# Performance work log

Hardware: AMD Instinct MI355X
Metric: run time of the kernel (lower is better)

Reference implementation:

```python
import jax, jax.numpy as jnp
import numpy as np

EMBED_DIM = 1024
NUM_HEADS = 16
HEAD_DIM = EMBED_DIM // NUM_HEADS
R = 16
LORA_ALPHA = 32
SCALING = LORA_ALPHA / R


def setup_inputs() -> dict:
    key = jax.random.key(0)
    ks = jax.random.split(key, 16)
    S, B, E = 2048, 4, EMBED_DIM
    def n(k, shape, scale=1.0):
        return jax.random.normal(k, shape, dtype=jnp.float32) * scale
    return {
        "x_q": n(ks[0], (S, B, E)),
        "x_k": n(ks[1], (S, B, E)),
        "x_v": n(ks[2], (S, B, E)),
        "Wq": n(ks[3], (E, E), 0.02),
        "bq": n(ks[4], (E,), 0.02),
        "Aq": n(ks[5], (E, R), 0.02),
        "Bq": n(ks[6], (R, E), 0.02),
        "Wk": n(ks[7], (E, E), 0.02),
        "bk": n(ks[8], (E,), 0.02),
        "Wv": n(ks[9], (E, E), 0.02),
        "bv": n(ks[10], (E,), 0.02),
        "Av": n(ks[11], (E, R), 0.02),
        "Bv": n(ks[12], (R, E), 0.02),
        "Wo": n(ks[13], (E, E), 0.02),
        "bo": n(ks[14], (E,), 0.02),
    }


def _lora_linear(x, W, b, A, B):
    # F.linear(x, W, b) + (x @ A) @ B * scaling
    return x @ W.T + b + ((x @ A) @ B) * SCALING


def reference(x_q, x_k, x_v, Wq, bq, Aq, Bq, Wk, bk, Wv, bv, Av, Bv, Wo, bo):
    S, Bsz, E = x_q.shape
    H, D = NUM_HEADS, HEAD_DIM
    q = _lora_linear(x_q, Wq, bq, Aq, Bq)      # [S, B, E]
    k = x_k @ Wk.T + bk                          # [S, B, E]
    v = _lora_linear(x_v, Wv, bv, Av, Bv)
    # [S, B, E] -> [B*H, S, D]
    q = q.reshape(S, Bsz * H, D).transpose(1, 0, 2)
    k = k.reshape(S, Bsz * H, D).transpose(1, 0, 2)
    v = v.reshape(S, Bsz * H, D).transpose(1, 0, 2)
    scores = jnp.einsum('nsd,ntd->nst', q, k) / (D ** 0.5)  # [B*H, S, S]
    attn = jax.nn.softmax(scores, axis=-1)
    out = jnp.einsum('nst,ntd->nsd', attn, v)                # [B*H, S, D]
    out = out.transpose(1, 0, 2).reshape(S, Bsz, E)
    return out @ Wo.T + bo
```

## Files before the change

### kernel.cpp

```cpp
#include <hip/hip_runtime.h>
#include <stdint.h>

#define S_LEN 2048
#define BSZ   4
#define EMB   1024
#define NH    16
#define HD    64
#define NHEADS (BSZ*NH)
#define M_ROWS (S_LEN*BSZ)
#define R_LORA 16

typedef unsigned short u16t;
typedef __bf16 bf16x8 __attribute__((ext_vector_type(8)));
typedef float  f32x4  __attribute__((ext_vector_type(4)));
typedef float  f32x16 __attribute__((ext_vector_type(16)));
typedef unsigned int uint2v __attribute__((ext_vector_type(2)));

#define QSCALE (0.125f * 1.44269504089f)

__device__ __forceinline__ u16t f2bf(float f){
  union { float f; uint32_t u; } v; v.f = f;
  uint32_t u = v.u;
  u += 0x7FFFu + ((u >> 16) & 1u);
  return (u16t)(u >> 16);
}

__device__ __forceinline__ uint32_t cvtpk(float a, float b){
  uint32_t r;
  asm("v_cvt_pk_bf16_f32 %0, %1, %2" : "=v"(r) : "v"(a), "v"(b));
  return r;
}

__device__ __forceinline__ void gload16(const void* g, void* l){
  __builtin_amdgcn_global_load_lds(
    (const __attribute__((address_space(1))) unsigned int*)g,
    (__attribute__((address_space(3))) unsigned int*)l, 16, 0, 0);
}

__device__ __forceinline__ int swz(int b){ return b ^ (((b >> 7) & 7) << 4); }

__global__ __launch_bounds__(256) void k_wprep4(
    const float* __restrict__ Wq, const float* __restrict__ Aq, const float* __restrict__ Bq,
    const float* __restrict__ Wk,
    const float* __restrict__ Wv, const float* __restrict__ Av, const float* __restrict__ Bv,
    const float* __restrict__ Wo,
    u16t* __restrict__ oq, u16t* __restrict__ ok, u16t* __restrict__ ov, u16t* __restrict__ oo){
  int which = blockIdx.y;
  const float* W = which==0?Wq : which==1?Wk : which==2?Wv : Wo;
  u16t* out      = which==0?oq : which==1?ok : which==2?ov : oo;
  int n = blockIdx.x, t = threadIdx.x;
  float4 wv = reinterpret_cast<const float4*>(W + (size_t)n*EMB)[t];
  float add[4] = {0.f, 0.f, 0.f, 0.f};
  if (which == 0 || which == 2){
    const float* A_ = which==0 ? Aq : Av;
    const float* B_ = which==0 ? Bq : Bv;
    float bcol[16];
    #pragma unroll
    for (int r = 0; r < 16; r++) bcol[r] = 2.0f * B_[(size_t)r*EMB + n];
    #pragma unroll
    for (int j = 0; j < 4; j++){
      const float4* ar = reinterpret_cast<const float4*>(A_ + (size_t)(4*t+j)*R_LORA);
      float4 a0 = ar[0], a1 = ar[1], a2 = ar[2], a3 = ar[3];
      add[j] = a0.x*bcol[0] + a0.y*bcol[1] + a0.z*bcol[2] + a0.w*bcol[3]
             + a1.x*bcol[4] + a1.y*bcol[5] + a1.z*bcol[6] + a1.w*bcol[7]
             + a2.x*bcol[8] + a2.y*bcol[9] + a2.z*bcol[10]+ a2.w*bcol[11]
             + a3.x*bcol[12]+ a3.y*bcol[13]+ a3.z*bcol[14]+ a3.w*bcol[15];
    }
  }
  float scale = (which == 0) ? QSCALE : 1.0f;
  ushort4 o = { f2bf((wv.x+add[0])*scale), f2bf((wv.y+add[1])*scale),
                f2bf((wv.z+add[2])*scale), f2bf((wv.w+add[3])*scale) };
  reinterpret_cast<ushort4*>(out + (size_t)n*EMB)[t] = o;
}

__global__ __launch_bounds__(256) void k_cvt3(
    const float* __restrict__ xq, const float* __restrict__ xk, const float* __restrict__ xv,
    u16t* __restrict__ oq, u16t* __restrict__ ok, u16t* __restrict__ ov){
  const float* x = blockIdx.y==0 ? xq : blockIdx.y==1 ? xk : xv;
  u16t* o        = blockIdx.y==0 ? oq : blockIdx.y==1 ? ok : ov;
  const int n = M_ROWS*EMB;
  int stride = gridDim.x * 256 * 4;
  for (int i = (blockIdx.x*256 + threadIdx.x)*4; i < n; i += stride){
    float4 v = *reinterpret_cast<const float4*>(x + i);
    ushort4 u = { f2bf(v.x), f2bf(v.y), f2bf(v.z), f2bf(v.w) };
    *reinterpret_cast<ushort4*>(o + i) = u;
  }
}

__device__ __forceinline__ void gemm_main(
    const u16t* __restrict__ Abase, const u16t* __restrict__ Bbase,
    u16t* smem, int t, int wr, int wc, int l15, int lg, f32x4 (&acc)[4][4]){
  int k0 = 0;
  auto stage = [&](int buf){
    u16t* d = smem + buf*16384;
    #pragma unroll
    for (int i = 0; i < 4; i++){
      int c = i*256 + t;
      int row = c >> 3, ch = c & 7;
      int srcch = ch ^ (row & 7);
      gload16(Abase + (size_t)row*EMB + k0 + srcch*8, d + c*8);
    }
    #pragma unroll
    for (int i = 0; i < 4; i++){
      int c = i*256 + t;
      int row = c >> 3, ch = c & 7;
      int srcch = ch ^ (row & 7);
      gload16(Bbase + (size_t)row*EMB + k0 + srcch*8, d + 8192 + c*8);
    }
    k0 += 64;
  };

  stage(0);
  __syncthreads();

  const int NK = EMB/64;
  for (int kt = 0; kt < NK; ++kt){
    int cur = kt & 1;
    if (kt+1 < NK) stage(cur^1);
    const char* Abuf = (const char*)(smem + cur*16384);
    const char* Bbuf = Abuf + 16384;
    #pragma unroll
    for (int kk = 0; kk < 2; kk++){
      bf16x8 af[4], bfr[4];
      #pragma unroll
      for (int i = 0; i < 4; i++){
        af[i]  = *reinterpret_cast<const bf16x8*>(
            Abuf + swz((wr*64 + i*16 + l15)*128 + kk*64 + lg*16));
        bfr[i] = *reinterpret_cast<const bf16x8*>(
            Bbuf + swz((wc*64 + i*16 + l15)*128 + kk*64 + lg*16));
      }
      __builtin_amdgcn_s_setprio(1);
      #pragma unroll
      for (int mi = 0; mi < 4; mi++)
        #pragma unroll
        for (int ni = 0; ni < 4; ni++)
          acc[mi][ni] = __builtin_amdgcn_mfma_f32_16x16x32_bf16(af[mi], bfr[ni], acc[mi][ni], 0, 0, 0);
      __builtin_amdgcn_s_setprio(0);
    }
    __syncthreads();
  }
}

__global__ __launch_bounds__(256) void k_gemm_qkv(
    const u16t* __restrict__ xqb, const u16t* __restrict__ xkb, const u16t* __restrict__ xvb,
    const u16t* __restrict__ Wqb, const u16t* __restrict__ Wkb, const u16t* __restrict__ Wvb,
    const float* __restrict__ bq, const float* __restrict__ bk, const float* __restrict__ bv,
    u16t* __restrict__ q_att, u16t* __restrict__ k_att, u16t* __restrict__ vT)
{
  __shared__ u16t smem[2*16384];
  int z = blockIdx.z;
  const u16t* A  = z==0 ? xqb : z==1 ? xkb : xvb;
  const u16t* Bw = z==0 ? Wqb : z==1 ? Wkb : Wvb;
  const float* bias = z==0 ? bq : z==1 ? bk : bv;
  float bscale = z==0 ? QSCALE : 1.0f;
  u16t* att = z==0 ? q_att : z==1 ? k_att : vT;

  int t = threadIdx.x;
  int lane = t & 63, w = t >> 6;
  int wr = w >> 1, wc = w & 1;
  int l15 = lane & 15, lg = lane >> 4;
  int m0 = blockIdx.x * 128;
  int n0 = blockIdx.y * 128;

  f32x4 acc[4][4];
  #pragma unroll
  for (int i = 0; i < 4; i++)
    #pragma unroll
    for (int j = 0; j < 4; j++)
      acc[i][j] = (f32x4){0.f, 0.f, 0.f, 0.f};

  gemm_main(A + (size_t)m0*EMB, Bw + (size_t)n0*EMB, smem, t, wr, wc, l15, lg, acc);

  float bval[4];
  #pragma unroll
  for (int ni = 0; ni < 4; ni++)
    bval[ni] = bias[n0 + wc*64 + ni*16 + l15] * bscale;

  if (z < 2){
    #pragma unroll
    for (int mi = 0; mi < 4; mi++)
      #pragma unroll
      for (int ni = 0; ni < 4; ni++)
        #pragma unroll
        for (int j = 0; j < 4; j++){
          int m_local = wr*64 + mi*16 + lg*4 + j;
          int n_local = wc*64 + ni*16 + l15;
          *(u16t*)((char*)smem + swz(m_local*256 + n_local*2)) = f2bf(acc[mi][ni][j] + bval[ni]);
        }
    __syncthreads();
    #pragma unroll
    for (int i = 0; i < 8; i++){
      int c = i*256 + t;
      int m_local = c >> 4, nch = c & 15;
      uint4 val = *(const uint4*)((const char*)smem + swz(m_local*256 + nch*16));
      int m = m0 + m_local;
      int s = m >> 2, b = m & 3;
      int n = n0 + nch*8;
      int h = n >> 6, d = n & 63;
      *(uint4*)&att[(size_t)((b*NH + h)*S_LEN + s)*HD + d] = val;
    }
  } else {
    #pragma unroll
    for (int mi = 0; mi < 4; mi++)
      #pragma unroll
      for (int ni = 0; ni < 4; ni++)
        #pragma unroll
        for (int j = 0; j < 4; j++){
          int m_local = wr*64 + mi*16 + lg*4 + j;
          int n_local = wc*64 + ni*16 + l15;
          *(u16t*)((char*)smem + swz(n_local*256 + m_local*2)) = f2bf(acc[mi][ni][j] + bval[ni]);
        }
    __syncthreads();
    #pragma unroll
    for (int i = 0; i < 8; i++){
      int u = i*256 + t;
      int dl = u >> 4, b = (u >> 2) & 3, sc = u & 3;
      u16t tmp[8];
      #pragma unroll
      for (int z2 = 0; z2 < 8; z2++)
        tmp[z2] = *(const u16t*)((const char*)smem + swz(dl*256 + ((sc*8+z2)*4 + b)*2));
      int n_glob = n0 + dl;
      int h = n_glob >> 6, d = n_glob & 63;
      int s0 = (m0 >> 2) + sc*8;
      *(uint4*)&att[((size_t)((b*NH + h)*HD + d))*S_LEN + s0] = *(const uint4*)tmp;
    }
  }
}

__global__ __launch_bounds__(256) void k_gemm_o(
    const u16t* __restrict__ A, const u16t* __restrict__ Bw,
    const float* __restrict__ bias, float* __restrict__ Cout)
{
  __shared__ u16t smem[2*16384];
  int t = threadIdx.x;
  int lane = t & 63, w = t >> 6;
  int wr = w >> 1, wc = w & 1;
  int l15 = lane & 15, lg = lane >> 4;
  int m0 = blockIdx.x * 128;
  int n0 = blockIdx.y * 128;

  f32x4 acc[4][4];
  #pragma unroll
  for (int i = 0; i < 4; i++)
    #pragma unroll
    for (int j = 0; j < 4; j++)
      acc[i][j] = (f32x4){0.f, 0.f, 0.f, 0.f};

  gemm_main(A + (size_t)m0*EMB, Bw + (size_t)n0*EMB, smem, t, wr, wc, l15, lg, acc);

  float bval[4];
  #pragma unroll
  for (int ni = 0; ni < 4; ni++)
    bval[ni] = bias[n0 + wc*64 + ni*16 + l15];

  #pragma unroll
  for (int mi = 0; mi < 4; mi++){
    #pragma unroll
    for (int j = 0; j < 4; j++){
      int m = m0 + wr*64 + mi*16 + lg*4 + j;
      #pragma unroll
      for (int ni = 0; ni < 4; ni++){
        int n = n0 + wc*64 + ni*16 + l15;
        Cout[(size_t)m*EMB + n] = acc[mi][ni][j] + bval[ni];
      }
    }
  }
}

__global__ __launch_bounds__(256) void k_attn(
    const u16t* __restrict__ Qa, const u16t* __restrict__ Ka,
    const u16t* __restrict__ VTa, u16t* __restrict__ Oa)
{
  __shared__ u16t smem[2*8192];
  int t = threadIdx.x;
  int lane = t & 63, w = t >> 6;
  int l31 = lane & 31, hi = lane >> 5;
  int head = blockIdx.x;
  int qw = blockIdx.y*128 + w*32;
  const u16t* Qh = Qa + (size_t)head * S_LEN * HD;
  const char* Khc = (const char*)(Ka + (size_t)head * S_LEN * HD);
  const char* VTc = (const char*)(VTa + (size_t)head * HD * S_LEN);

  bf16x8 qf[4];
  #pragma unroll
  for (int ds = 0; ds < 4; ds++)
    qf[ds] = *reinterpret_cast<const bf16x8*>(
        Qh + (size_t)(qw + l31)*HD + ds*16 + hi*8);

  bf16x8 ones;
  { union { uint32_t u[4]; bf16x8 v; } o;
    o.u[0]=o.u[1]=o.u[2]=o.u[3]=0x3F803F80u; ones = o.v; }

  f32x16 oacc[2], lacc;
  oacc[0] = (f32x16)(0.f); oacc[1] = (f32x16)(0.f); lacc = (f32x16)(0.f);

  auto stage = [&](int buf, int key0){
    char* Kd = (char*)smem + buf*16384;
    char* Vd = Kd + 8192;
    #pragma unroll
    for (int i = 0; i < 2; i++){
      int c = i*256 + t;
      gload16(Khc + (size_t)key0*128 + swz(c*16), Kd + c*16);
    }
    #pragma unroll
    for (int i = 0; i < 2; i++){
      int c = i*256 + t;
      int tb = swz(c*16);
      gload16(VTc + (size_t)(tb>>7)*(S_LEN*2) + key0*2 + (tb&127), Vd + c*16);
    }
  };

  stage(0, 0);
  __syncthreads();

  const int NT = S_LEN/64;
  for (int nt = 0; nt < NT; ++nt){
    int cur = nt & 1;
    if (nt+1 < NT) stage(cur^1, (nt+1)*64);
    const char* Kb = (const char*)smem + cur*16384;
    const char* Vb = Kb + 8192;

    f32x16 sacc[2];
    sacc[0] = (f32x16)(0.f); sacc[1] = (f32x16)(0.f);
    __builtin_amdgcn_s_setprio(1);
    #pragma unroll
    for (int blk = 0; blk < 2; blk++){
      #pragma unroll
      for (int ds = 0; ds < 4; ds++){
        bf16x8 kf = *reinterpret_cast<const bf16x8*>(Kb + swz((blk*32 + l31)*128 + ds*32 + hi*16));
        sacc[blk] = __builtin_amdgcn_mfma_f32_32x32x16_bf16(kf, qf[ds], sacc[blk], 0,0,0);
      }
    }
    __builtin_amdgcn_s_setprio(0);

    #pragma unroll
    for (int blk = 0; blk < 2; blk++)
      #pragma unroll
      for (int r = 0; r < 16; r++)
        sacc[blk][r] = __builtin_amdgcn_exp2f(sacc[blk][r]);

    bf16x8 pa[4];
    #pragma unroll
    for (int blk = 0; blk < 2; blk++){
      #pragma unroll
      for (int kl = 0; kl < 2; kl++){
        union { uint32_t u[4]; bf16x8 v; } fr;
        #pragma unroll
        for (int i = 0; i < 2; i++){
          uint32_t x = cvtpk(sacc[blk][kl*8 + 2*i],     sacc[blk][kl*8 + 2*i + 1]);
          uint32_t y = cvtpk(sacc[blk][kl*8 + 4 + 2*i], sacc[blk][kl*8 + 4 + 2*i + 1]);
          uint2v r = __builtin_amdgcn_permlane32_swap(x, y, false, false);
          fr.u[i]   = r.x;
          fr.u[i+2] = r.y;
        }
        pa[blk*2 + kl] = fr.v;
      }
    }

    __builtin_amdgcn_s_setprio(1);
    #pragma unroll
    for (int dblk = 0; dblk < 2; dblk++){
      #pragma unroll
      for (int ks = 0; ks < 4; ks++){
        bf16x8 vf = *reinterpret_cast<const bf16x8*>(Vb + swz((dblk*32 + l31)*128 + ks*32 + hi*16));
        oacc[dblk] = __builtin_amdgcn_mfma_f32_32x32x16_bf16(vf, pa[ks], oacc[dblk], 0,0,0);
      }
    }
    #pragma unroll
    for (int ks = 0; ks < 4; ks++)
      lacc = __builtin_amdgcn_mfma_f32_32x32x16_bf16(ones, pa[ks], lacc, 0,0,0);
    __builtin_amdgcn_s_setprio(0);
    __syncthreads();
  }

  float inv = 1.0f / lacc[0];
  #pragma unroll
  for (int dblk = 0; dblk < 2; dblk++){
    #pragma unroll
    for (int rp = 0; rp < 8; rp++){
      int reg = 2*rp;
      int d = dblk*32 + (reg&3) + 8*(reg>>2) + 4*hi;
      uint32_t wv = cvtpk(oacc[dblk][reg]*inv, oacc[dblk][reg+1]*inv);
      *(uint32_t*)((char*)smem + swz((w*32 + l31)*128 + d*2)) = wv;
    }
  }
  __syncthreads();
  int b = head >> 4, h = head & 15;
  #pragma unroll
  for (int i = 0; i < 4; i++){
    int c = i*256 + t;
    int row = c >> 3;
    int col = c & 7;
    uint4 val = *(const uint4*)((const char*)smem + swz(row*128 + col*16));
    int q = blockIdx.y*128 + row;
    *(uint4*)(Oa + (size_t)(q*BSZ + b)*EMB + h*HD + col*8) = val;
  }
}

extern "C" void kernel_launch(void* const* d_in, const int* in_sizes, int n_in,
                              void* d_out, int out_size, void* d_ws, size_t ws_size,
                              hipStream_t stream) {
  const float* x_q = (const float*)d_in[0];
  const float* x_k = (const float*)d_in[1];
  const float* x_v = (const float*)d_in[2];
  const float* Wq  = (const float*)d_in[3];
  const float* bq  = (const float*)d_in[4];
  const float* Aq  = (const float*)d_in[5];
  const float* Bq  = (const float*)d_in[6];
  const float* Wk  = (const float*)d_in[7];
  const float* bk  = (const float*)d_in[8];
  const float* Wv  = (const float*)d_in[9];
  const float* bv  = (const float*)d_in[10];
  const float* Av  = (const float*)d_in[11];
  const float* Bv  = (const float*)d_in[12];
  const float* Wo  = (const float*)d_in[13];
  const float* bo  = (const float*)d_in[14];
  float* out = (float*)d_out;

  char* ws = (char*)d_ws;
  size_t off = 0;
  auto alloc = [&](size_t bytes){
    void* p = ws + off; off += (bytes + 255) & ~(size_t)255; return p;
  };
  u16t* xqb   = (u16t*)alloc((size_t)M_ROWS*EMB*2);
  u16t* xkb   = (u16t*)alloc((size_t)M_ROWS*EMB*2);
  u16t* xvb   = (u16t*)alloc((size_t)M_ROWS*EMB*2);
  u16t* q_att = (u16t*)alloc((size_t)M_ROWS*EMB*2);
  u16t* k_att = (u16t*)alloc((size_t)M_ROWS*EMB*2);
  u16t* vT    = (u16t*)alloc((size_t)M_ROWS*EMB*2);
  u16t* Wqb = (u16t*)alloc((size_t)EMB*EMB*2);
  u16t* Wkb = (u16t*)alloc((size_t)EMB*EMB*2);
  u16t* Wvb = (u16t*)alloc((size_t)EMB*EMB*2);
  u16t* Wob = (u16t*)alloc((size_t)EMB*EMB*2);
  (void)ws_size; (void)in_sizes; (void)n_in; (void)out_size;

  k_wprep4<<<dim3(EMB, 4), 256, 0, stream>>>(Wq, Aq, Bq, Wk, Wv, Av, Bv, Wo,
                                             Wqb, Wkb, Wvb, Wob);
  k_cvt3<<<dim3(2048, 3), 256, 0, stream>>>(x_q, x_k, x_v, xqb, xkb, xvb);

  k_gemm_qkv<<<dim3(M_ROWS/128, EMB/128, 3), 256, 0, stream>>>(
      xqb, xkb, xvb, Wqb, Wkb, Wvb, bq, bk, bv, q_att, k_att, vT);

  k_attn<<<dim3(NHEADS, S_LEN/128), 256, 0, stream>>>(q_att, k_att, vT, xqb);

  k_gemm_o<<<dim3(M_ROWS/128, EMB/128), 256, 0, stream>>>(xqb, Wob, bo, out);
}
```

Before: 235.3 us.

## Rewrite QKV GEMM as 256x256-tile, 8-wave kernel with interleaved LDS pipeline

Replaces the 128x128, 4-wave QKV projection GEMM with a 256x256-tile, 512-thread kernel that uses 128 KB of dynamic LDS for double-buffered A/B tiles. The main loop interleaves fragment loads, MFMA batches and the next tile's global-to-LDS loads, using raw s_barrier and vmcnt waits instead of __syncthreads. Block indices are remapped to a swizzled order. The larger tile raises arithmetic intensity and overlaps loads with compute, at the cost of fewer blocks (384), higher register pressure and reliance on hand-placed waitcnt counts for correctness. The shared gemm_main helper is inlined into the output-projection kernel, which is otherwise unchanged.

```diff
diff --git a/kernel.cpp b/kernel.cpp
--- a/kernel.cpp
+++ b/kernel.cpp
@@ -17,6 +17,10 @@
 typedef unsigned int uint2v __attribute__((ext_vector_type(2)));
 
 #define QSCALE (0.125f * 1.44269504089f)
+
+#define BARRIER_RAW  asm volatile("s_barrier" ::: "memory")
+#define VMCNT8       asm volatile("s_waitcnt vmcnt(8)" ::: "memory")
+#define VMCNT0       asm volatile("s_waitcnt vmcnt(0)" ::: "memory")
 
 __device__ __forceinline__ u16t f2bf(float f){
   union { float f; uint32_t u; } v; v.f = f;
@@ -87,142 +91,178 @@
   }
 }
 
-__device__ __forceinline__ void gemm_main(
-    const u16t* __restrict__ Abase, const u16t* __restrict__ Bbase,
-    u16t* smem, int t, int wr, int wc, int l15, int lg, f32x4 (&acc)[4][4]){
-  int k0 = 0;
-  auto stage = [&](int buf){
-    u16t* d = smem + buf*16384;
-    #pragma unroll
-    for (int i = 0; i < 4; i++){
-      int c = i*256 + t;
-      int row = c >> 3, ch = c & 7;
-      int srcch = ch ^ (row & 7);
-      gload16(Abase + (size_t)row*EMB + k0 + srcch*8, d + c*8);
-    }
-    #pragma unroll
-    for (int i = 0; i < 4; i++){
-      int c = i*256 + t;
-      int row = c >> 3, ch = c & 7;
-      int srcch = ch ^ (row & 7);
-      gload16(Bbase + (size_t)row*EMB + k0 + srcch*8, d + 8192 + c*8);
-    }
-    k0 += 64;
-  };
-
-  stage(0);
-  __syncthreads();
-
-  const int NK = EMB/64;
-  for (int kt = 0; kt < NK; ++kt){
-    int cur = kt & 1;
-    if (kt+1 < NK) stage(cur^1);
-    const char* Abuf = (const char*)(smem + cur*16384);
-    const char* Bbuf = Abuf + 16384;
-    #pragma unroll
-    for (int kk = 0; kk < 2; kk++){
-      bf16x8 af[4], bfr[4];
-      #pragma unroll
-      for (int i = 0; i < 4; i++){
-        af[i]  = *reinterpret_cast<const bf16x8*>(
-            Abuf + swz((wr*64 + i*16 + l15)*128 + kk*64 + lg*16));
-        bfr[i] = *reinterpret_cast<const bf16x8*>(
-            Bbuf + swz((wc*64 + i*16 + l15)*128 + kk*64 + lg*16));
-      }
-      __builtin_amdgcn_s_setprio(1);
-      #pragma unroll
-      for (int mi = 0; mi < 4; mi++)
-        #pragma unroll
-        for (int ni = 0; ni < 4; ni++)
-          acc[mi][ni] = __builtin_amdgcn_mfma_f32_16x16x32_bf16(af[mi], bfr[ni], acc[mi][ni], 0, 0, 0);
-      __builtin_amdgcn_s_setprio(0);
-    }
-    __syncthreads();
-  }
-}
-
-__global__ __launch_bounds__(256) void k_gemm_qkv(
+__global__ __launch_bounds__(512, 2) void k_gemm_qkv8(
     const u16t* __restrict__ xqb, const u16t* __restrict__ xkb, const u16t* __restrict__ xvb,
     const u16t* __restrict__ Wqb, const u16t* __restrict__ Wkb, const u16t* __restrict__ Wvb,
     const float* __restrict__ bq, const float* __restrict__ bk, const float* __restrict__ bv,
     u16t* __restrict__ q_att, u16t* __restrict__ k_att, u16t* __restrict__ vT)
 {
-  __shared__ u16t smem[2*16384];
-  int z = blockIdx.z;
-  const u16t* A  = z==0 ? xqb : z==1 ? xkb : xvb;
-  const u16t* Bw = z==0 ? Wqb : z==1 ? Wkb : Wvb;
-  const float* bias = z==0 ? bq : z==1 ? bk : bv;
-  float bscale = z==0 ? QSCALE : 1.0f;
-  u16t* att = z==0 ? q_att : z==1 ? k_att : vT;
+  extern __shared__ u16t smem[];
+  int lin = blockIdx.x + 32*(blockIdx.y + 4*blockIdx.z);
+  int nl  = (lin & 7)*48 + (lin >> 3);
+  int bx = nl & 31, rest = nl >> 5;
+  int by = rest & 3, bz = rest >> 2;
+
+  const u16t* Ap = bz==0 ? xqb : bz==1 ? xkb : xvb;
+  const u16t* Bp = bz==0 ? Wqb : bz==1 ? Wkb : Wvb;
+  const float* bias = bz==0 ? bq : bz==1 ? bk : bv;
+  float bscale = bz==0 ? QSCALE : 1.0f;
 
   int t = threadIdx.x;
-  int lane = t & 63, w = t >> 6;
-  int wr = w >> 1, wc = w & 1;
+  int lane = t & 63, wid = t >> 6;
+  int wr = wid >> 2, wc = wid & 3;
   int l15 = lane & 15, lg = lane >> 4;
-  int m0 = blockIdx.x * 128;
-  int n0 = blockIdx.y * 128;
-
-  f32x4 acc[4][4];
-  #pragma unroll
-  for (int i = 0; i < 4; i++)
+  int m0 = bx * 256;
+  int n0 = by * 256;
+  const u16t* Ag = Ap + (size_t)m0*EMB;
+  const u16t* Bg = Bp + (size_t)n0*EMB;
+
+  auto stageA = [&](int buf, int k, int h){
+    const u16t* src = Ag + (size_t)(h*128)*EMB + k*64;
+    char* dst = (char*)smem + buf*65536 + h*16384;
+    #pragma unroll
+    for (int i = 0; i < 2; i++){
+      int c = i*512 + t;
+      int row = c >> 3, ch = c & 7;
+      gload16(src + (size_t)row*EMB + (ch ^ (row & 7))*8, dst + c*16);
+    }
+  };
+  auto stageB = [&](int buf, int k, int h){
+    const u16t* src = Bg + (size_t)(h*128)*EMB + k*64;
+    char* dst = (char*)smem + buf*65536 + 32768 + h*16384;
+    #pragma unroll
+    for (int i = 0; i < 2; i++){
+      int c = i*512 + t;
+      int row = c >> 3, ch = c & 7;
+      gload16(src + (size_t)row*EMB + (ch ^ (row & 7))*8, dst + c*16);
+    }
+  };
+
+  f32x4 acc[8][4];
+  #pragma unroll
+  for (int i = 0; i < 8; i++)
     #pragma unroll
     for (int j = 0; j < 4; j++)
       acc[i][j] = (f32x4){0.f, 0.f, 0.f, 0.f};
 
-  gemm_main(A + (size_t)m0*EMB, Bw + (size_t)n0*EMB, smem, t, wr, wc, l15, lg, acc);
+  bf16x8 af[4][2];
+  bf16x8 bfr[4][2];
+
+  auto ldA = [&](int buf, int miBase){
+    const char* base = (const char*)smem + buf*65536 + wr*16384;
+    #pragma unroll
+    for (int m2 = 0; m2 < 4; m2++)
+      #pragma unroll
+      for (int kk = 0; kk < 2; kk++)
+        af[m2][kk] = *reinterpret_cast<const bf16x8*>(
+            base + swz(((miBase+m2)*16 + l15)*128 + kk*64 + lg*16));
+  };
+  auto ldB2 = [&](int buf, int niBase){
+    const char* base = (const char*)smem + buf*65536 + 32768 + (wc>>1)*16384;
+    #pragma unroll
+    for (int n2 = 0; n2 < 2; n2++)
+      #pragma unroll
+      for (int kk = 0; kk < 2; kk++)
+        bfr[niBase+n2][kk] = *reinterpret_cast<const bf16x8*>(
+            base + swz(((wc&1)*64 + (niBase+n2)*16 + l15)*128 + kk*64 + lg*16));
+  };
+  auto mma8 = [&](int miBase, int niBase){
+    __builtin_amdgcn_s_setprio(1);
+    #pragma unroll
+    for (int kk = 0; kk < 2; kk++)
+      #pragma unroll
+      for (int m2 = 0; m2 < 4; m2++)
+        #pragma unroll
+        for (int n2 = 0; n2 < 2; n2++)
+          acc[miBase+m2][niBase+n2] = __builtin_amdgcn_mfma_f32_16x16x32_bf16(
+              af[m2][kk], bfr[niBase+n2][kk], acc[miBase+m2][niBase+n2], 0, 0, 0);
+    __builtin_amdgcn_s_setprio(0);
+  };
+
+  stageA(0, 0, 0); stageA(0, 0, 1); stageB(0, 0, 0); stageB(0, 0, 1);
+  stageB(1, 1, 0); stageB(1, 1, 1); stageA(1, 1, 0); stageA(1, 1, 1);
+  VMCNT8;
+  BARRIER_RAW;
+
+  const int NT = EMB/64;
+  for (int kt = 0; kt < NT; kt += 2){
+    #pragma unroll
+    for (int half = 0; half < 2; half++){
+      int bc = half;
+      int ktile = kt + half;
+      int tn = ktile + 2;
+      bool hasNext = (tn < NT);
+      ldB2(bc, 0);
+      ldA(bc, 0);
+      mma8(0, 0);
+      ldB2(bc, 2);
+      mma8(0, 2);
+      BARRIER_RAW;
+      if (hasNext){ stageB(bc, tn, 0); stageB(bc, tn, 1); }
+      ldA(bc, 4);
+      mma8(4, 0);
+      BARRIER_RAW;
+      if (hasNext){ stageA(bc, tn, 0); stageA(bc, tn, 1); }
+      mma8(4, 2);
+      if (hasNext){ VMCNT8; } else { VMCNT0; }
+      BARRIER_RAW;
+    }
+  }
 
   float bval[4];
   #pragma unroll
   for (int ni = 0; ni < 4; ni++)
     bval[ni] = bias[n0 + wc*64 + ni*16 + l15] * bscale;
 
-  if (z < 2){
-    #pragma unroll
-    for (int mi = 0; mi < 4; mi++)
+  if (bz < 2){
+    #pragma unroll
+    for (int mi = 0; mi < 8; mi++)
       #pragma unroll
       for (int ni = 0; ni < 4; ni++)
         #pragma unroll
         for (int j = 0; j < 4; j++){
-          int m_local = wr*64 + mi*16 + lg*4 + j;
+          int m_local = wr*128 + mi*16 + lg*4 + j;
           int n_local = wc*64 + ni*16 + l15;
-          *(u16t*)((char*)smem + swz(m_local*256 + n_local*2)) = f2bf(acc[mi][ni][j] + bval[ni]);
+          *(u16t*)((char*)smem + swz(m_local*512 + n_local*2)) = f2bf(acc[mi][ni][j] + bval[ni]);
         }
     __syncthreads();
     #pragma unroll
-    for (int i = 0; i < 8; i++){
-      int c = i*256 + t;
-      int m_local = c >> 4, nch = c & 15;
-      uint4 val = *(const uint4*)((const char*)smem + swz(m_local*256 + nch*16));
+    for (int i = 0; i < 16; i++){
+      int c = i*512 + t;
+      int m_local = c >> 5, nch = c & 31;
+      uint4 val = *(const uint4*)((const char*)smem + swz(m_local*512 + nch*16));
       int m = m0 + m_local;
       int s = m >> 2, b = m & 3;
       int n = n0 + nch*8;
       int h = n >> 6, d = n & 63;
+      u16t* att = bz==0 ? q_att : k_att;
       *(uint4*)&att[(size_t)((b*NH + h)*S_LEN + s)*HD + d] = val;
     }
   } else {
     #pragma unroll
-    for (int mi = 0; mi < 4; mi++)
+    for (int mi = 0; mi < 8; mi++)
       #pragma unroll
       for (int ni = 0; ni < 4; ni++)
         #pragma unroll
         for (int j = 0; j < 4; j++){
-          int m_local = wr*64 + mi*16 + lg*4 + j;
+          int m_local = wr*128 + mi*16 + lg*4 + j;
           int n_local = wc*64 + ni*16 + l15;
-          *(u16t*)((char*)smem + swz(n_local*256 + m_local*2)) = f2bf(acc[mi][ni][j] + bval[ni]);
+          *(u16t*)((char*)smem + swz(n_local*512 + m_local*2)) = f2bf(acc[mi][ni][j] + bval[ni]);
         }
     __syncthreads();
     #pragma unroll
-    for (int i = 0; i < 8; i++){
-      int u = i*256 + t;
-      int dl = u >> 4, b = (u >> 2) & 3, sc = u & 3;
+    for (int i = 0; i < 16; i++){
+      int c = i*512 + t;
+      int dl = c >> 5, rem = c & 31;
+      int b = rem >> 3, sc = rem & 7;
       u16t tmp[8];
       #pragma unroll
       for (int z2 = 0; z2 < 8; z2++)
-        tmp[z2] = *(const u16t*)((const char*)smem + swz(dl*256 + ((sc*8+z2)*4 + b)*2));
+        tmp[z2] = *(const u16t*)((const char*)smem + swz(dl*512 + ((sc*8+z2)*4 + b)*2));
       int n_glob = n0 + dl;
       int h = n_glob >> 6, d = n_glob & 63;
       int s0 = (m0 >> 2) + sc*8;
-      *(uint4*)&att[((size_t)((b*NH + h)*HD + d))*S_LEN + s0] = *(const uint4*)tmp;
+      *(uint4*)&vT[((size_t)((b*NH + h)*HD + d))*S_LEN + s0] = *(const uint4*)tmp;
     }
   }
 }
@@ -239,6 +279,26 @@
   int m0 = blockIdx.x * 128;
   int n0 = blockIdx.y * 128;
 
+  const u16t* Abase = A  + (size_t)m0*EMB;
+  const u16t* Bbase = Bw + (size_t)n0*EMB;
+  int k0 = 0;
+  auto stage = [&](int buf){
+    u16t* d = smem + buf*16384;
+    #pragma unroll
+    for (int i = 0; i < 4; i++){
+      int c = i*256 + t;
+      int row = c >> 3, ch = c & 7;
+      gload16(Abase + (size_t)row*EMB + k0 + (ch ^ (row & 7))*8, d + c*8);
+    }
+    #pragma unroll
+    for (int i = 0; i < 4; i++){
+      int c = i*256 + t;
+      int row = c >> 3, ch = c & 7;
+      gload16(Bbase + (size_t)row*EMB + k0 + (ch ^ (row & 7))*8, d + 8192 + c*8);
+    }
+    k0 += 64;
+  };
+
   f32x4 acc[4][4];
   #pragma unroll
   for (int i = 0; i < 4; i++)
@@ -246,7 +306,35 @@
     for (int j = 0; j < 4; j++)
       acc[i][j] = (f32x4){0.f, 0.f, 0.f, 0.f};
 
-  gemm_main(A + (size_t)m0*EMB, Bw + (size_t)n0*EMB, smem, t, wr, wc, l15, lg, acc);
+  stage(0);
+  __syncthreads();
+
+  const int NK = EMB/64;
+  for (int kt = 0; kt < NK; ++kt){
+    int cur = kt & 1;
+    if (kt+1 < NK) stage(cur^1);
+    const char* Abuf = (const char*)(smem + cur*16384);
+    const char* Bbuf = Abuf + 16384;
+    #pragma unroll
+    for (int kk = 0; kk < 2; kk++){
+      bf16x8 af[4], bfr[4];
+      #pragma unroll
+      for (int i = 0; i < 4; i++){
+        af[i]  = *reinterpret_cast<const bf16x8*>(
+            Abuf + swz((wr*64 + i*16 + l15)*128 + kk*64 + lg*16));
+        bfr[i] = *reinterpret_cast<const bf16x8*>(
+            Bbuf + swz((wc*64 + i*16 + l15)*128 + kk*64 + lg*16));
+      }
+      __builtin_amdgcn_s_setprio(1);
+      #pragma unroll
+      for (int mi = 0; mi < 4; mi++)
+        #pragma unroll
+        for (int ni = 0; ni < 4; ni++)
+          acc[mi][ni] = __builtin_amdgcn_mfma_f32_16x16x32_bf16(af[mi], bfr[ni], acc[mi][ni], 0, 0, 0);
+      __builtin_amdgcn_s_setprio(0);
+    }
+    __syncthreads();
+  }
 
   float bval[4];
   #pragma unroll
@@ -438,7 +526,7 @@
                                              Wqb, Wkb, Wvb, Wob);
   k_cvt3<<<dim3(2048, 3), 256, 0, stream>>>(x_q, x_k, x_v, xqb, xkb, xvb);
 
-  k_gemm_qkv<<<dim3(M_ROWS/128, EMB/128, 3), 256, 0, stream>>>(
+  k_gemm_qkv8<<<dim3(M_ROWS/256, EMB/256, 3), 512, 131072, stream>>>(
       xqb, xkb, xvb, Wqb, Wkb, Wvb, bq, bk, bv, q_att, k_att, vT);
 
   k_attn<<<dim3(NHEADS, S_LEN/128), 256, 0, stream>>>(q_att, k_att, vT, xqb);
```

Measured after the change: 251.1 us. +6.7%, slower.
